# Performance work log

Measured on AMD Instinct MI355X. Metric: run time of the kernel, lower is better.

The kernel has to match this reference:

```python
import math
import jax, jax.numpy as jnp
import numpy as np

NUM_EXPERTS = 8
TOP_K = 2
HIDDEN = 1024
INTERMEDIATE = 4096
CAPACITY_FACTOR = 1.0


def setup_inputs() -> dict:
    key = jax.random.key(0)
    k1, k2, k3, k4, k5, k6 = jax.random.split(key, 6)
    T = 8192
    hidden_states = jax.random.normal(k1, (T, HIDDEN), dtype=jnp.float32)
    # router affinities (already softmax-normalized in the real pipeline; uniform here is fine for correctness)
    expert_affinities = jax.random.uniform(k2, (T, NUM_EXPERTS), dtype=jnp.float32)
    expert_index = jax.random.randint(k3, (T, TOP_K), 0, NUM_EXPERTS, dtype=jnp.int32)
    scale = 0.02
    gate_w = jax.random.normal(k4, (NUM_EXPERTS, HIDDEN, INTERMEDIATE), dtype=jnp.float32) * scale
    up_w = jax.random.normal(k5, (NUM_EXPERTS, HIDDEN, INTERMEDIATE), dtype=jnp.float32) * scale
    down_w = jax.random.normal(k6, (NUM_EXPERTS, INTERMEDIATE, HIDDEN), dtype=jnp.float32) * scale
    return {"hidden_states": hidden_states, "expert_affinities": expert_affinities,
            "gate_w": gate_w, "up_w": up_w, "down_w": down_w, "expert_index": expert_index}


def reference(hidden_states, expert_affinities, gate_w, up_w, down_w, expert_index):
    T, H = hidden_states.shape
    E, K = NUM_EXPERTS, TOP_K
    C = min(math.ceil(T * K * CAPACITY_FACTOR / E), T)  # expert capacity (static)

    # top_k-hot expert mask (T, E)
    expert_mask = jax.nn.one_hot(expert_index, E, dtype=jnp.float32).sum(axis=1)
    # 1-indexed position of each token within each expert's queue
    position_in_expert = jnp.cumsum(expert_mask, axis=0)
    # capacity-based token dropping
    expert_mask = jnp.where(position_in_expert > C, 0.0, expert_mask)

    # masked (and L1-normalized) affinities of chosen experts
    aff_masked = jnp.where(expert_mask == 0, 0.0, expert_affinities)
    denom = jnp.maximum(jnp.sum(jnp.abs(aff_masked), axis=1, keepdims=True), 1e-12)
    aff_masked = aff_masked / denom  # normalize_top_k_affinities=True

    # flattened slot index per (token, expert): expert e occupies slots [e*C, (e+1)*C)
    offsets = jnp.arange(E, dtype=jnp.float32) * C
    pos_off = position_in_expert + offsets[None, :]
    pos_off = jnp.where(expert_mask == 0, 0.0, pos_off)

    # (T, K) slot index (1-based; 0 == dropped)
    perm_idx = jnp.take_along_axis(pos_off, expert_index, axis=1).astype(jnp.int32)

    # invert permutation: slot -> token (1-based; slot 0 collects all dropped tokens, then discarded)
    tok_ids = jnp.broadcast_to((jnp.arange(T, dtype=jnp.int32) + 1)[:, None], (T, K)).reshape(-1)
    assign = jnp.zeros(E * C + 1, dtype=jnp.int32).at[perm_idx.reshape(-1)].set(tok_ids)
    assign = assign[1:].reshape(E, C) - 1
    assign = jnp.maximum(assign, 0)          # empty slots read token 0 (output unused)
    perm_idx = jnp.maximum(perm_idx - 1, 0)  # dropped tokens read slot 0 (affinity == 0)

    # gather tokens into per-expert blocks and run grouped GLU MLP
    x_e = hidden_states[assign]  # (E, C, H)
    gate = jax.nn.silu(jnp.einsum('ech,ehi->eci', x_e, gate_w))
    inter = gate * jnp.einsum('ech,ehi->eci', x_e, up_w)  # (E, C, I)
    out_e = jnp.einsum('eci,eih->ech', inter, down_w)      # (E, C, H)
    permuted_output = out_e.reshape(E * C, H)

    # combine: gather each token's top_k expert outputs weighted by masked affinities
    out_k = permuted_output[perm_idx]                                   # (T, K, H)
    aff_k = jnp.take_along_axis(aff_masked, expert_index, axis=1)       # (T, K)
    return jnp.sum(out_k * aff_k[:, :, None], axis=1)
```

## Files before the change

kernel.cpp:

```cpp
#include <hip/hip_runtime.h>
#include <stdint.h>

#define T_TOK 8192
#define HID   1024
#define INTER 4096
#define NE    8
#define TOPK  2
#define CAP   2048
#define EC    (NE * CAP)


typedef __attribute__((ext_vector_type(8))) short bf16x8;
typedef __attribute__((ext_vector_type(4))) float f32x4;

static __device__ __forceinline__ unsigned short f2bf(float f) {
    union { float f; unsigned u; } a; a.f = f;
    unsigned r = a.u + 0x7FFFu + ((a.u >> 16) & 1u);
    return (unsigned short)(r >> 16);
}
static __device__ __forceinline__ float bf2f(unsigned short b) {
    union { unsigned u; float f; } a; a.u = ((unsigned)b) << 16;
    return a.f;
}

static __device__ __forceinline__ void gload(const unsigned short* g, unsigned short* l) {
    __builtin_amdgcn_global_load_lds((__attribute__((address_space(1))) void*)(uintptr_t)g,
                                     (__attribute__((address_space(3))) void*)l, 16, 0, 0);
}

#define BAR() do { asm volatile("" ::: "memory"); __builtin_amdgcn_s_barrier(); asm volatile("" ::: "memory"); } while (0)
#define WAITVM(N) asm volatile("s_waitcnt vmcnt(" #N ")" ::: "memory")

__global__ __launch_bounds__(512) void route_kernel(const int* __restrict__ eidx,
                                                    int* __restrict__ perm,
                                                    int* __restrict__ assign) {
    int tid = threadIdx.x;
    for (int i = tid; i < EC; i += 512) assign[i] = 0;
    __syncthreads();
    int e = tid >> 6;
    int lane = tid & 63;
    const int TPL = T_TOK / 64;
    int t0 = lane * TPL;
    int cnt = 0;
    for (int t = t0; t < t0 + TPL; ++t) {
        int e0 = eidx[t * 2], e1 = eidx[t * 2 + 1];
        cnt += (e0 == e) + (e1 == e);
    }
    int incl = cnt;
    #pragma unroll
    for (int off = 1; off < 64; off <<= 1) {
        int n = __shfl_up(incl, off, 64);
        if (lane >= off) incl += n;
    }
    int run = incl - cnt;
    for (int t = t0; t < t0 + TPL; ++t) {
        int e0 = eidx[t * 2], e1 = eidx[t * 2 + 1];
        int c = (e0 == e) + (e1 == e);
        if (c) {
            run += c;
            int pos = run;
            bool keep = (pos <= CAP);
            int pi = keep ? (pos + e * CAP) : 0;
            if (e0 == e) perm[t * 2]     = pi;
            if (e1 == e) perm[t * 2 + 1] = pi;
            if (keep) assign[pi - 1] = t;
        }
    }
}

__global__ __launch_bounds__(256) void transpose_cvt2(const float* __restrict__ in0,
                                                      unsigned short* __restrict__ out0,
                                                      const float* __restrict__ in1,
                                                      unsigned short* __restrict__ out1) {
    __shared__ unsigned short tile[64][68];
    int z = blockIdx.z;
    const float* in = (z < 8) ? in0 : in1;
    unsigned short* out = (z < 8) ? out0 : out1;
    int e = z & 7;
    const int R = HID, Cc = INTER;
    const float* inp = in + (size_t)e * R * Cc;
    unsigned short* outp = out + (size_t)e * R * Cc;
    int c0 = blockIdx.x * 64, r0 = blockIdx.y * 64;
    int t = threadIdx.x;
    int x = t & 15;
    int ry = t >> 4;
    #pragma unroll
    for (int j = 0; j < 4; ++j) {
        int row = ry + 16 * j;
        float4 v = *(const float4*)(inp + (size_t)(r0 + row) * Cc + c0 + 4 * x);
        ushort4 o;
        o.x = f2bf(v.x); o.y = f2bf(v.y); o.z = f2bf(v.z); o.w = f2bf(v.w);
        *(ushort4*)&tile[row][4 * x] = o;
    }
    __syncthreads();
    #pragma unroll
    for (int j = 0; j < 4; ++j) {
        int oc = ry + 16 * j;
        ushort4 o;
        o.x = tile[4 * x + 0][oc];
        o.y = tile[4 * x + 1][oc];
        o.z = tile[4 * x + 2][oc];
        o.w = tile[4 * x + 3][oc];
        *(ushort4*)(outp + (size_t)(c0 + oc) * R + r0 + 4 * x) = o;
    }
}

__global__ __launch_bounds__(256) void transpose_cvt(const float* __restrict__ in,
                                                     unsigned short* __restrict__ out,
                                                     int R, int Cc) {
    __shared__ unsigned short tile[64][68];
    int e = blockIdx.z;
    const float* inp = in + (size_t)e * R * Cc;
    unsigned short* outp = out + (size_t)e * R * Cc;
    int c0 = blockIdx.x * 64, r0 = blockIdx.y * 64;
    int t = threadIdx.x;
    int x = t & 15;
    int ry = t >> 4;
    #pragma unroll
    for (int j = 0; j < 4; ++j) {
        int row = ry + 16 * j;
        float4 v = *(const float4*)(inp + (size_t)(r0 + row) * Cc + c0 + 4 * x);
        ushort4 o;
        o.x = f2bf(v.x); o.y = f2bf(v.y); o.z = f2bf(v.z); o.w = f2bf(v.w);
        *(ushort4*)&tile[row][4 * x] = o;
    }
    __syncthreads();
    #pragma unroll
    for (int j = 0; j < 4; ++j) {
        int oc = ry + 16 * j;
        ushort4 o;
        o.x = tile[4 * x + 0][oc];
        o.y = tile[4 * x + 1][oc];
        o.z = tile[4 * x + 2][oc];
        o.w = tile[4 * x + 3][oc];
        *(ushort4*)(outp + (size_t)(c0 + oc) * R + r0 + 4 * x) = o;
    }
}

__global__ __launch_bounds__(256) void gather_cvt(const float* __restrict__ hs,
                                                  const int* __restrict__ assign,
                                                  unsigned short* __restrict__ xe) {
    int s = blockIdx.x;
    int tok = assign[s];
    const float* src = hs + (size_t)tok * HID;
    unsigned short* dst = xe + (size_t)s * HID;
    int h = threadIdx.x * 4;
    float4 v = *(const float4*)(src + h);
    ushort4 o;
    o.x = f2bf(v.x); o.y = f2bf(v.y); o.z = f2bf(v.z); o.w = f2bf(v.w);
    *(ushort4*)(dst + h) = o;
}


#define BUFE 12288

#define MFMA16(ACC, O, B0, B1) \
    _Pragma("unroll") \
    for (int mi = 0; mi < 8; ++mi) { \
        ACC[mi][O]     = __builtin_amdgcn_mfma_f32_16x16x32_bf16(aF[mi], B0, ACC[mi][O], 0, 0, 0); \
        ACC[mi][O + 1] = __builtin_amdgcn_mfma_f32_16x16x32_bf16(aF[mi], B1, ACC[mi][O + 1], 0, 0, 0); \
    }

#define LOAD_AF(rd) \
    _Pragma("unroll") \
    for (int mi = 0; mi < 8; ++mi) aF[mi] = *(const bf16x8*)((rd) + aRd + mi * 512);

__global__ __launch_bounds__(256, 2) void gateup_gemm(const unsigned short* __restrict__ Xe,
                                                      const unsigned short* __restrict__ WgT,
                                                      const unsigned short* __restrict__ WuT,
                                                      unsigned short* __restrict__ interB) {
    extern __shared__ __align__(16) unsigned short smemU[];
    const int K = HID;
    const int NT = K / 32;

    int e  = blockIdx.x;
    int m0 = blockIdx.y * 256;
    int n0 = blockIdx.z * 64;

    int tid = threadIdx.x;
    int lane = tid & 63, w = tid >> 6;
    int lm = lane & 15, hi = lane >> 4;
    int wm = w >> 1, wn = w & 1;

    const int swz  = (hi ^ ((lm >> 1) & 3)) << 3;
    const int aRd  = (wm * 128 + lm) * 32 + swz;
    const int r1Rd = 8192  + (wn * 32 + lm) * 32 + swz;
    const int r2Rd = 10240 + (wn * 32 + lm) * 32 + swz;

    int sr = lane >> 2;
    int sc = ((lane & 3) ^ ((lane >> 3) & 3)) << 3;
    const unsigned short* aS = Xe  + ((size_t)e * CAP   + m0 + w * 64 + sr) * K + sc;
    const unsigned short* gS = WgT + ((size_t)e * INTER + n0 + w * 16 + sr) * K + sc;
    const unsigned short* uS = WuT + ((size_t)e * INTER + n0 + w * 16 + sr) * K + sc;
    const int dA = w * 2048;
    const int dG = 8192  + w * 512;
    const int dU = 10240 + w * 512;

    f32x4 zero = {0.f, 0.f, 0.f, 0.f};
    f32x4 accG[8][2], accU[8][2];
    #pragma unroll
    for (int i = 0; i < 8; ++i) {
        accG[i][0] = zero; accG[i][1] = zero;
        accU[i][0] = zero; accU[i][1] = zero;
    }

    unsigned short* p0 = smemU;
    unsigned short* p1 = smemU + BUFE;
    unsigned short* p2 = smemU + 2 * BUFE;

    {
        #pragma unroll
        for (int j = 0; j < 4; ++j) gload(aS + (size_t)j * 16 * K, p0 + dA + j * 512);
        gload(gS, p0 + dG); gload(uS, p0 + dU);
        #pragma unroll
        for (int j = 0; j < 4; ++j) gload(aS + (size_t)j * 16 * K + 32, p1 + dA + j * 512);
        gload(gS + 32, p1 + dG); gload(uS + 32, p1 + dU);
        WAITVM(6);
        BAR();
    }

    bf16x8 aF[8];
    int gk = 64;
    for (int t = 0; t < NT - 2; ++t) {
        const unsigned short* rd = p0;
        unsigned short* wr = p2;
        LOAD_AF(rd);
        bf16x8 g0 = *(const bf16x8*)(rd + r1Rd);
        bf16x8 g1 = *(const bf16x8*)(rd + r1Rd + 512);
        bf16x8 u0 = *(const bf16x8*)(rd + r2Rd);
        bf16x8 u1 = *(const bf16x8*)(rd + r2Rd + 512);
        #pragma unroll
        for (int j = 0; j < 4; ++j) gload(aS + (size_t)j * 16 * K + gk, wr + dA + j * 512);
        gload(gS + gk, wr + dG);
        gload(uS + gk, wr + dU);
        WAITVM(6);
        BAR();
        __builtin_amdgcn_s_setprio(1);
        MFMA16(accG, 0, g0, g1);
        MFMA16(accU, 0, u0, u1);
        __builtin_amdgcn_s_setprio(0);
        BAR();
        unsigned short* tmp = p0; p0 = p1; p1 = p2; p2 = tmp;
        gk += 32;
    }
    {
        const unsigned short* rd = p0;
        LOAD_AF(rd);
        bf16x8 g0 = *(const bf16x8*)(rd + r1Rd);
        bf16x8 g1 = *(const bf16x8*)(rd + r1Rd + 512);
        bf16x8 u0 = *(const bf16x8*)(rd + r2Rd);
        bf16x8 u1 = *(const bf16x8*)(rd + r2Rd + 512);
        WAITVM(0);
        BAR();
        MFMA16(accG, 0, g0, g1);
        MFMA16(accU, 0, u0, u1);
        BAR();
    }
    {
        const unsigned short* rd = p1;
        LOAD_AF(rd);
        bf16x8 g0 = *(const bf16x8*)(rd + r1Rd);
        bf16x8 g1 = *(const bf16x8*)(rd + r1Rd + 512);
        bf16x8 u0 = *(const bf16x8*)(rd + r2Rd);
        bf16x8 u1 = *(const bf16x8*)(rd + r2Rd + 512);
        MFMA16(accG, 0, g0, g1);
        MFMA16(accU, 0, u0, u1);
    }

    __syncthreads();
    unsigned short* bounce = smemU;
    #pragma unroll
    for (int mi = 0; mi < 8; ++mi)
        #pragma unroll
        for (int nf = 0; nf < 2; ++nf) {
            f32x4 g4 = accG[mi][nf], u4 = accU[mi][nf];
            #pragma unroll
            for (int r = 0; r < 4; ++r) {
                int row = wm * 128 + mi * 16 + (lane >> 4) * 4 + r;
                int col = wn * 32 + nf * 16 + lm;
                float g = g4[r];
                float s = g / (1.f + __expf(-g)) * u4[r];
                bounce[row * 72 + col] = f2bf(s);
            }
        }
    __syncthreads();
    {
        unsigned short* Op = interB + ((size_t)e * CAP + m0) * INTER + n0;
        int rr = tid >> 3, cc = (tid & 7) * 8;
        #pragma unroll
        for (int j = 0; j < 8; ++j) {
            int row = rr + 32 * j;
            bf16x8 v = *(const bf16x8*)&bounce[row * 72 + cc];
            *(bf16x8*)(Op + (size_t)row * INTER + cc) = v;
        }
    }
}

__global__ __launch_bounds__(256, 2) void down_gemm(const unsigned short* __restrict__ interB,
                                                    const unsigned short* __restrict__ WdT,
                                                    unsigned short* __restrict__ pout) {
    extern __shared__ __align__(16) unsigned short smemU[];
    const int K = INTER;
    const int NT = K / 32;

    int e  = blockIdx.x;
    int m0 = blockIdx.y * 256;
    int n0 = blockIdx.z * 128;

    int tid = threadIdx.x;
    int lane = tid & 63, w = tid >> 6;
    int lm = lane & 15, hi = lane >> 4;
    int wm = w >> 1, wn = w & 1;

    const int swz  = (hi ^ ((lm >> 1) & 3)) << 3;
    const int aRd  = (wm * 128 + lm) * 32 + swz;
    const int r1Rd = 8192  + (wn * 32 + lm) * 32 + swz;
    const int r2Rd = 10240 + (wn * 32 + lm) * 32 + swz;

    int sr = lane >> 2;
    int sc = ((lane & 3) ^ ((lane >> 3) & 3)) << 3;
    const unsigned short* aS = interB + ((size_t)e * CAP + m0 + w * 64 + sr) * K + sc;
    int rb1 = (w >> 1) * 64 + (w & 1) * 16;
    const unsigned short* b1S = WdT + ((size_t)e * HID + n0 + rb1 + sr) * K + sc;
    const unsigned short* b2S = WdT + ((size_t)e * HID + n0 + rb1 + 32 + sr) * K + sc;
    const int dA = w * 2048;
    const int d1 = 8192  + w * 512;
    const int d2 = 10240 + w * 512;

    f32x4 zero = {0.f, 0.f, 0.f, 0.f};
    f32x4 acc[8][4];
    #pragma unroll
    for (int i = 0; i < 8; ++i)
        #pragma unroll
        for (int j = 0; j < 4; ++j) acc[i][j] = zero;

    unsigned short* p0 = smemU;
    unsigned short* p1 = smemU + BUFE;
    unsigned short* p2 = smemU + 2 * BUFE;

    {
        #pragma unroll
        for (int j = 0; j < 4; ++j) gload(aS + (size_t)j * 16 * K, p0 + dA + j * 512);
        gload(b1S, p0 + d1); gload(b2S, p0 + d2);
        #pragma unroll
        for (int j = 0; j < 4; ++j) gload(aS + (size_t)j * 16 * K + 32, p1 + dA + j * 512);
        gload(b1S + 32, p1 + d1); gload(b2S + 32, p1 + d2);
        WAITVM(6);
        BAR();
    }

    bf16x8 aF[8];
    int gk = 64;
    for (int t = 0; t < NT - 2; ++t) {
        const unsigned short* rd = p0;
        unsigned short* wr = p2;
        LOAD_AF(rd);
        bf16x8 b0 = *(const bf16x8*)(rd + r1Rd);
        bf16x8 b1 = *(const bf16x8*)(rd + r1Rd + 512);
        bf16x8 b2 = *(const bf16x8*)(rd + r2Rd);
        bf16x8 b3 = *(const bf16x8*)(rd + r2Rd + 512);
        #pragma unroll
        for (int j = 0; j < 4; ++j) gload(aS + (size_t)j * 16 * K + gk, wr + dA + j * 512);
        gload(b1S + gk, wr + d1);
        gload(b2S + gk, wr + d2);
        WAITVM(6);
        BAR();
        __builtin_amdgcn_s_setprio(1);
        MFMA16(acc, 0, b0, b1);
        MFMA16(acc, 2, b2, b3);
        __builtin_amdgcn_s_setprio(0);
        BAR();
        unsigned short* tmp = p0; p0 = p1; p1 = p2; p2 = tmp;
        gk += 32;
    }
    {
        const unsigned short* rd = p0;
        LOAD_AF(rd);
        bf16x8 b0 = *(const bf16x8*)(rd + r1Rd);
        bf16x8 b1 = *(const bf16x8*)(rd + r1Rd + 512);
        bf16x8 b2 = *(const bf16x8*)(rd + r2Rd);
        bf16x8 b3 = *(const bf16x8*)(rd + r2Rd + 512);
        WAITVM(0);
        BAR();
        MFMA16(acc, 0, b0, b1);
        MFMA16(acc, 2, b2, b3);
        BAR();
    }
    {
        const unsigned short* rd = p1;
        LOAD_AF(rd);
        bf16x8 b0 = *(const bf16x8*)(rd + r1Rd);
        bf16x8 b1 = *(const bf16x8*)(rd + r1Rd + 512);
        bf16x8 b2 = *(const bf16x8*)(rd + r2Rd);
        bf16x8 b3 = *(const bf16x8*)(rd + r2Rd + 512);
        MFMA16(acc, 0, b0, b1);
        MFMA16(acc, 2, b2, b3);
    }

    unsigned short* bounce = smemU;
    unsigned short* Op = pout + ((size_t)e * CAP + m0) * HID + n0;
    int rr = tid >> 3, c8 = tid & 7;
    int colp = c8 * 8;
    #pragma unroll
    for (int R = 0; R < 2; ++R) {
        __syncthreads();
        #pragma unroll
        for (int mi = 0; mi < 8; ++mi)
            #pragma unroll
            for (int nf = 0; nf < 2; ++nf) {
                f32x4 a4 = acc[mi][2 * R + nf];
                #pragma unroll
                for (int r = 0; r < 4; ++r) {
                    int row = wm * 128 + mi * 16 + hi * 4 + r;
                    int col = wn * 32 + nf * 16 + lm;
                    bounce[row * 72 + col] = f2bf(a4[r]);
                }
            }
        __syncthreads();
        int gcol = (colp >> 5) * 64 + R * 32 + (colp & 31);
        #pragma unroll
        for (int j = 0; j < 8; ++j) {
            int row = rr + 32 * j;
            bf16x8 v = *(const bf16x8*)&bounce[row * 72 + colp];
            *(bf16x8*)(Op + (size_t)row * HID + gcol) = v;
        }
    }
}

__global__ __launch_bounds__(256) void combine_kernel(const float* __restrict__ aff,
                                                      const int* __restrict__ eidx,
                                                      const int* __restrict__ perm,
                                                      const unsigned short* __restrict__ pout,
                                                      float* __restrict__ out) {
    int t = blockIdx.x;
    int e0 = eidx[t * 2], e1 = eidx[t * 2 + 1];
    int p0 = perm[t * 2], p1 = perm[t * 2 + 1];
    bool k0 = p0 > 0, k1 = p1 > 0;
    float a0 = aff[t * NE + e0], a1 = aff[t * NE + e1];
    float denom = (k0 ? fabsf(a0) : 0.f) + ((e1 != e0 && k1) ? fabsf(a1) : 0.f);
    denom = fmaxf(denom, 1e-12f);
    float w0 = k0 ? a0 / denom : 0.f;
    float w1 = k1 ? a1 / denom : 0.f;
    int s0 = k0 ? p0 - 1 : 0;
    int s1 = k1 ? p1 - 1 : 0;
    int h = threadIdx.x * 4;
    ushort4 v0 = *(const ushort4*)(pout + (size_t)s0 * HID + h);
    ushort4 v1 = *(const ushort4*)(pout + (size_t)s1 * HID + h);
    float4 o;
    o.x = w0 * bf2f(v0.x) + w1 * bf2f(v1.x);
    o.y = w0 * bf2f(v0.y) + w1 * bf2f(v1.y);
    o.z = w0 * bf2f(v0.z) + w1 * bf2f(v1.z);
    o.w = w0 * bf2f(v0.w) + w1 * bf2f(v1.w);
    *(float4*)(out + (size_t)t * HID + h) = o;
}

extern "C" void kernel_launch(void* const* d_in, const int* in_sizes, int n_in,
                              void* d_out, int out_size, void* d_ws, size_t ws_size,
                              hipStream_t stream) {
    (void)in_sizes; (void)n_in; (void)out_size; (void)ws_size;
    const float* hs   = (const float*)d_in[0];
    const float* aff  = (const float*)d_in[1];
    const float* gw   = (const float*)d_in[2];
    const float* uw   = (const float*)d_in[3];
    const float* dw   = (const float*)d_in[4];
    const int*   eidx = (const int*)d_in[5];
    float* out = (float*)d_out;

    char* ws = (char*)d_ws;
    unsigned short* WgT    = (unsigned short*)(ws);
    unsigned short* WuT    = (unsigned short*)(ws + ((size_t)64  << 20));
    unsigned short* WdT    = (unsigned short*)(ws + ((size_t)128 << 20));
    unsigned short* Xe     = (unsigned short*)(ws + ((size_t)192 << 20));
    unsigned short* interB = (unsigned short*)(ws + ((size_t)224 << 20));
    unsigned short* pout   = (unsigned short*)(ws + ((size_t)352 << 20));
    int*            perm   = (int*)           (ws + ((size_t)416 << 20));
    int*            assign = perm + (T_TOK * TOPK);

    static int attr_set = 0;
    if (!attr_set) {
        (void)hipFuncSetAttribute((const void*)gateup_gemm,
                                  hipFuncAttributeMaxDynamicSharedMemorySize, 73728);
        (void)hipFuncSetAttribute((const void*)down_gemm,
                                  hipFuncAttributeMaxDynamicSharedMemorySize, 73728);
        attr_set = 1;
    }

    route_kernel<<<1, 512, 0, stream>>>(eidx, perm, assign);
    transpose_cvt2<<<dim3(INTER / 64, HID / 64, 16), 256, 0, stream>>>(uw, WuT, gw, WgT);
    transpose_cvt<<<dim3(HID / 64, INTER / 64, NE), 256, 0, stream>>>(dw, WdT, INTER, HID);
    gather_cvt<<<EC, 256, 0, stream>>>(hs, assign, Xe);
    gateup_gemm<<<dim3(8, 8, 64), 256, 73728, stream>>>(Xe, WgT, WuT, interB);
    down_gemm<<<dim3(8, 8, 8), 256, 73728, stream>>>(interB, WdT, pout);
    combine_kernel<<<T_TOK, 256, 0, stream>>>(aff, eidx, perm, pout, out);
}
```

Baseline: 911.5 us.

## Load A operand directly to registers, stage only weights through LDS

```diff
diff --git a/kernel.cpp b/kernel.cpp
--- a/kernel.cpp
+++ b/kernel.cpp
@@ -152,19 +152,6 @@
 }
 
 
-#define BUFE 12288
-
-#define MFMA16(ACC, O, B0, B1) \
-    _Pragma("unroll") \
-    for (int mi = 0; mi < 8; ++mi) { \
-        ACC[mi][O]     = __builtin_amdgcn_mfma_f32_16x16x32_bf16(aF[mi], B0, ACC[mi][O], 0, 0, 0); \
-        ACC[mi][O + 1] = __builtin_amdgcn_mfma_f32_16x16x32_bf16(aF[mi], B1, ACC[mi][O + 1], 0, 0, 0); \
-    }
-
-#define LOAD_AF(rd) \
-    _Pragma("unroll") \
-    for (int mi = 0; mi < 8; ++mi) aF[mi] = *(const bf16x8*)((rd) + aRd + mi * 512);
-
 __global__ __launch_bounds__(256, 2) void gateup_gemm(const unsigned short* __restrict__ Xe,
                                                       const unsigned short* __restrict__ WgT,
                                                       const unsigned short* __restrict__ WuT,
@@ -183,18 +170,15 @@
     int wm = w >> 1, wn = w & 1;
 
     const int swz  = (hi ^ ((lm >> 1) & 3)) << 3;
-    const int aRd  = (wm * 128 + lm) * 32 + swz;
-    const int r1Rd = 8192  + (wn * 32 + lm) * 32 + swz;
-    const int r2Rd = 10240 + (wn * 32 + lm) * 32 + swz;
+    const int bOff = (wn * 32 + lm) * 32 + swz;
 
     int sr = lane >> 2;
     int sc = ((lane & 3) ^ ((lane >> 3) & 3)) << 3;
-    const unsigned short* aS = Xe  + ((size_t)e * CAP   + m0 + w * 64 + sr) * K + sc;
     const unsigned short* gS = WgT + ((size_t)e * INTER + n0 + w * 16 + sr) * K + sc;
     const unsigned short* uS = WuT + ((size_t)e * INTER + n0 + w * 16 + sr) * K + sc;
-    const int dA = w * 2048;
-    const int dG = 8192  + w * 512;
-    const int dU = 10240 + w * 512;
+    const int dW = w * 512;
+
+    const unsigned short* aP = Xe + ((size_t)e * CAP + m0 + wm * 128 + lm) * K + hi * 8;
 
     f32x4 zero = {0.f, 0.f, 0.f, 0.f};
     f32x4 accG[8][2], accU[8][2];
@@ -204,68 +188,84 @@
         accU[i][0] = zero; accU[i][1] = zero;
     }
 
-    unsigned short* p0 = smemU;
-    unsigned short* p1 = smemU + BUFE;
-    unsigned short* p2 = smemU + 2 * BUFE;
-
+    int bR = 0, bM = 4096, bS = 8192;
+    bf16x8 aC[8], aN[8];
+
+    gload(gS,      smemU + bR + dW);  gload(uS,      smemU + bR + 2048 + dW);
+    gload(gS + 32, smemU + bM + dW);  gload(uS + 32, smemU + bM + 2048 + dW);
+    #pragma unroll
+    for (int mi = 0; mi < 8; ++mi) aC[mi] = *(const bf16x8*)(aP + mi * 16 * K);
+    WAITVM(10);
+    BAR();
+
+#define GU_TILE(AC, AN, tkc) \
+    { \
+        gload(gS + (tkc) + 64, smemU + bS + dW); \
+        gload(uS + (tkc) + 64, smemU + bS + 2048 + dW); \
+        _Pragma("unroll") \
+        for (int mi = 0; mi < 8; ++mi) \
+            AN[mi] = *(const bf16x8*)(aP + mi * 16 * K + (tkc) + 32); \
+        WAITVM(10); \
+        BAR(); \
+        { \
+            bf16x8 g0 = *(const bf16x8*)(smemU + bR + bOff); \
+            bf16x8 g1 = *(const bf16x8*)(smemU + bR + bOff + 512); \
+            bf16x8 u0 = *(const bf16x8*)(smemU + bR + 2048 + bOff); \
+            bf16x8 u1 = *(const bf16x8*)(smemU + bR + 2048 + bOff + 512); \
+            __builtin_amdgcn_s_setprio(1); \
+            _Pragma("unroll") \
+            for (int mi = 0; mi < 8; ++mi) { \
+                accG[mi][0] = __builtin_amdgcn_mfma_f32_16x16x32_bf16(AC[mi], g0, accG[mi][0], 0, 0, 0); \
+                accG[mi][1] = __builtin_amdgcn_mfma_f32_16x16x32_bf16(AC[mi], g1, accG[mi][1], 0, 0, 0); \
+                accU[mi][0] = __builtin_amdgcn_mfma_f32_16x16x32_bf16(AC[mi], u0, accU[mi][0], 0, 0, 0); \
+                accU[mi][1] = __builtin_amdgcn_mfma_f32_16x16x32_bf16(AC[mi], u1, accU[mi][1], 0, 0, 0); \
+            } \
+            __builtin_amdgcn_s_setprio(0); \
+        } \
+        BAR(); \
+        int _bt = bR; bR = bM; bM = bS; bS = _bt; \
+    }
+
+    int tk = 0;
+    for (int t = 0; t < NT - 2; t += 2) {
+        GU_TILE(aC, aN, tk);
+        GU_TILE(aN, aC, tk + 32);
+        tk += 64;
+    }
     {
         #pragma unroll
-        for (int j = 0; j < 4; ++j) gload(aS + (size_t)j * 16 * K, p0 + dA + j * 512);
-        gload(gS, p0 + dG); gload(uS, p0 + dU);
-        #pragma unroll
-        for (int j = 0; j < 4; ++j) gload(aS + (size_t)j * 16 * K + 32, p1 + dA + j * 512);
-        gload(gS + 32, p1 + dG); gload(uS + 32, p1 + dU);
-        WAITVM(6);
+        for (int mi = 0; mi < 8; ++mi) aN[mi] = *(const bf16x8*)(aP + mi * 16 * K + tk + 32);
+        WAITVM(8);
         BAR();
-    }
-
-    bf16x8 aF[8];
-    int gk = 64;
-    for (int t = 0; t < NT - 2; ++t) {
-        const unsigned short* rd = p0;
-        unsigned short* wr = p2;
-        LOAD_AF(rd);
-        bf16x8 g0 = *(const bf16x8*)(rd + r1Rd);
-        bf16x8 g1 = *(const bf16x8*)(rd + r1Rd + 512);
-        bf16x8 u0 = *(const bf16x8*)(rd + r2Rd);
-        bf16x8 u1 = *(const bf16x8*)(rd + r2Rd + 512);
-        #pragma unroll
-        for (int j = 0; j < 4; ++j) gload(aS + (size_t)j * 16 * K + gk, wr + dA + j * 512);
-        gload(gS + gk, wr + dG);
-        gload(uS + gk, wr + dU);
-        WAITVM(6);
+        bf16x8 g0 = *(const bf16x8*)(smemU + bR + bOff);
+        bf16x8 g1 = *(const bf16x8*)(smemU + bR + bOff + 512);
+        bf16x8 u0 = *(const bf16x8*)(smemU + bR + 2048 + bOff);
+        bf16x8 u1 = *(const bf16x8*)(smemU + bR + 2048 + bOff + 512);
+        #pragma unroll
+        for (int mi = 0; mi < 8; ++mi) {
+            accG[mi][0] = __builtin_amdgcn_mfma_f32_16x16x32_bf16(aC[mi], g0, accG[mi][0], 0, 0, 0);
+            accG[mi][1] = __builtin_amdgcn_mfma_f32_16x16x32_bf16(aC[mi], g1, accG[mi][1], 0, 0, 0);
+            accU[mi][0] = __builtin_amdgcn_mfma_f32_16x16x32_bf16(aC[mi], u0, accU[mi][0], 0, 0, 0);
+            accU[mi][1] = __builtin_amdgcn_mfma_f32_16x16x32_bf16(aC[mi], u1, accU[mi][1], 0, 0, 0);
+        }
         BAR();
-        __builtin_amdgcn_s_setprio(1);
-        MFMA16(accG, 0, g0, g1);
-        MFMA16(accU, 0, u0, u1);
-        __builtin_amdgcn_s_setprio(0);
-        BAR();
-        unsigned short* tmp = p0; p0 = p1; p1 = p2; p2 = tmp;
-        gk += 32;
+        int _bt = bR; bR = bM; bM = bS; bS = _bt;
     }
     {
-        const unsigned short* rd = p0;
-        LOAD_AF(rd);
-        bf16x8 g0 = *(const bf16x8*)(rd + r1Rd);
-        bf16x8 g1 = *(const bf16x8*)(rd + r1Rd + 512);
-        bf16x8 u0 = *(const bf16x8*)(rd + r2Rd);
-        bf16x8 u1 = *(const bf16x8*)(rd + r2Rd + 512);
         WAITVM(0);
-        BAR();
-        MFMA16(accG, 0, g0, g1);
-        MFMA16(accU, 0, u0, u1);
-        BAR();
-    }
-    {
-        const unsigned short* rd = p1;
-        LOAD_AF(rd);
-        bf16x8 g0 = *(const bf16x8*)(rd + r1Rd);
-        bf16x8 g1 = *(const bf16x8*)(rd + r1Rd + 512);
-        bf16x8 u0 = *(const bf16x8*)(rd + r2Rd);
-        bf16x8 u1 = *(const bf16x8*)(rd + r2Rd + 512);
-        MFMA16(accG, 0, g0, g1);
-        MFMA16(accU, 0, u0, u1);
-    }
+        bf16x8 g0 = *(const bf16x8*)(smemU + bR + bOff);
+        bf16x8 g1 = *(const bf16x8*)(smemU + bR + bOff + 512);
+        bf16x8 u0 = *(const bf16x8*)(smemU + bR + 2048 + bOff);
+        bf16x8 u1 = *(const bf16x8*)(smemU + bR + 2048 + bOff + 512);
+        #pragma unroll
+        for (int mi = 0; mi < 8; ++mi) {
+            accG[mi][0] = __builtin_amdgcn_mfma_f32_16x16x32_bf16(aN[mi], g0, accG[mi][0], 0, 0, 0);
+            accG[mi][1] = __builtin_amdgcn_mfma_f32_16x16x32_bf16(aN[mi], g1, accG[mi][1], 0, 0, 0);
+            accU[mi][0] = __builtin_amdgcn_mfma_f32_16x16x32_bf16(aN[mi], u0, accU[mi][0], 0, 0, 0);
+            accU[mi][1] = __builtin_amdgcn_mfma_f32_16x16x32_bf16(aN[mi], u1, accU[mi][1], 0, 0, 0);
+        }
+    }
+#undef GU_TILE
 
     __syncthreads();
     unsigned short* bounce = smemU;
@@ -276,7 +276,7 @@
             f32x4 g4 = accG[mi][nf], u4 = accU[mi][nf];
             #pragma unroll
             for (int r = 0; r < 4; ++r) {
-                int row = wm * 128 + mi * 16 + (lane >> 4) * 4 + r;
+                int row = wm * 128 + mi * 16 + hi * 4 + r;
                 int col = wn * 32 + nf * 16 + lm;
                 float g = g4[r];
                 float s = g / (1.f + __expf(-g)) * u4[r];
@@ -304,8 +304,8 @@
     const int NT = K / 32;
 
     int e  = blockIdx.x;
-    int m0 = blockIdx.y * 256;
-    int n0 = blockIdx.z * 128;
+    int n0 = blockIdx.y * 128;
+    int m0 = blockIdx.z * 256;
 
     int tid = threadIdx.x;
     int lane = tid & 63, w = tid >> 6;
@@ -313,19 +313,16 @@
     int wm = w >> 1, wn = w & 1;
 
     const int swz  = (hi ^ ((lm >> 1) & 3)) << 3;
-    const int aRd  = (wm * 128 + lm) * 32 + swz;
-    const int r1Rd = 8192  + (wn * 32 + lm) * 32 + swz;
-    const int r2Rd = 10240 + (wn * 32 + lm) * 32 + swz;
+    const int bOff = (wn * 32 + lm) * 32 + swz;
 
     int sr = lane >> 2;
     int sc = ((lane & 3) ^ ((lane >> 3) & 3)) << 3;
-    const unsigned short* aS = interB + ((size_t)e * CAP + m0 + w * 64 + sr) * K + sc;
     int rb1 = (w >> 1) * 64 + (w & 1) * 16;
     const unsigned short* b1S = WdT + ((size_t)e * HID + n0 + rb1 + sr) * K + sc;
     const unsigned short* b2S = WdT + ((size_t)e * HID + n0 + rb1 + 32 + sr) * K + sc;
-    const int dA = w * 2048;
-    const int d1 = 8192  + w * 512;
-    const int d2 = 10240 + w * 512;
+    const int dW = w * 512;
+
+    const unsigned short* aP = interB + ((size_t)e * CAP + m0 + wm * 128 + lm) * K + hi * 8;
 
     f32x4 zero = {0.f, 0.f, 0.f, 0.f};
     f32x4 acc[8][4];
@@ -334,68 +331,84 @@
         #pragma unroll
         for (int j = 0; j < 4; ++j) acc[i][j] = zero;
 
-    unsigned short* p0 = smemU;
-    unsigned short* p1 = smemU + BUFE;
-    unsigned short* p2 = smemU + 2 * BUFE;
-
+    int bR = 0, bM = 4096, bS = 8192;
+    bf16x8 aC[8], aN[8];
+
+    gload(b1S,      smemU + bR + dW);  gload(b2S,      smemU + bR + 2048 + dW);
+    gload(b1S + 32, smemU + bM + dW);  gload(b2S + 32, smemU + bM + 2048 + dW);
+    #pragma unroll
+    for (int mi = 0; mi < 8; ++mi) aC[mi] = *(const bf16x8*)(aP + mi * 16 * K);
+    WAITVM(10);
+    BAR();
+
+#define DN_TILE(AC, AN, tkc) \
+    { \
+        gload(b1S + (tkc) + 64, smemU + bS + dW); \
+        gload(b2S + (tkc) + 64, smemU + bS + 2048 + dW); \
+        _Pragma("unroll") \
+        for (int mi = 0; mi < 8; ++mi) \
+            AN[mi] = *(const bf16x8*)(aP + mi * 16 * K + (tkc) + 32); \
+        WAITVM(10); \
+        BAR(); \
+        { \
+            bf16x8 b0 = *(const bf16x8*)(smemU + bR + bOff); \
+            bf16x8 b1 = *(const bf16x8*)(smemU + bR + bOff + 512); \
+            bf16x8 b2 = *(const bf16x8*)(smemU + bR + 2048 + bOff); \
+            bf16x8 b3 = *(const bf16x8*)(smemU + bR + 2048 + bOff + 512); \
+            __builtin_amdgcn_s_setprio(1); \
+            _Pragma("unroll") \
+            for (int mi = 0; mi < 8; ++mi) { \
+                acc[mi][0] = __builtin_amdgcn_mfma_f32_16x16x32_bf16(AC[mi], b0, acc[mi][0], 0, 0, 0); \
+                acc[mi][1] = __builtin_amdgcn_mfma_f32_16x16x32_bf16(AC[mi], b1, acc[mi][1], 0, 0, 0); \
+                acc[mi][2] = __builtin_amdgcn_mfma_f32_16x16x32_bf16(AC[mi], b2, acc[mi][2], 0, 0, 0); \
+                acc[mi][3] = __builtin_amdgcn_mfma_f32_16x16x32_bf16(AC[mi], b3, acc[mi][3], 0, 0, 0); \
+            } \
+            __builtin_amdgcn_s_setprio(0); \
+        } \
+        BAR(); \
+        int _bt = bR; bR = bM; bM = bS; bS = _bt; \
+    }
+
+    int tk = 0;
+    for (int t = 0; t < NT - 2; t += 2) {
+        DN_TILE(aC, aN, tk);
+        DN_TILE(aN, aC, tk + 32);
+        tk += 64;
+    }
     {
         #pragma unroll
-        for (int j = 0; j < 4; ++j) gload(aS + (size_t)j * 16 * K, p0 + dA + j * 512);
-        gload(b1S, p0 + d1); gload(b2S, p0 + d2);
-        #pragma unroll
-        for (int j = 0; j < 4; ++j) gload(aS + (size_t)j * 16 * K + 32, p1 + dA + j * 512);
-        gload(b1S + 32, p1 + d1); gload(b2S + 32, p1 + d2);
-        WAITVM(6);
+        for (int mi = 0; mi < 8; ++mi) aN[mi] = *(const bf16x8*)(aP + mi * 16 * K + tk + 32);
+        WAITVM(8);
         BAR();
-    }
-
-    bf16x8 aF[8];
-    int gk = 64;
-    for (int t = 0; t < NT - 2; ++t) {
-        const unsigned short* rd = p0;
-        unsigned short* wr = p2;
-        LOAD_AF(rd);
-        bf16x8 b0 = *(const bf16x8*)(rd + r1Rd);
-        bf16x8 b1 = *(const bf16x8*)(rd + r1Rd + 512);
-        bf16x8 b2 = *(const bf16x8*)(rd + r2Rd);
-        bf16x8 b3 = *(const bf16x8*)(rd + r2Rd + 512);
-        #pragma unroll
-        for (int j = 0; j < 4; ++j) gload(aS + (size_t)j * 16 * K + gk, wr + dA + j * 512);
-        gload(b1S + gk, wr + d1);
-        gload(b2S + gk, wr + d2);
-        WAITVM(6);
+        bf16x8 b0 = *(const bf16x8*)(smemU + bR + bOff);
+        bf16x8 b1 = *(const bf16x8*)(smemU + bR + bOff + 512);
+        bf16x8 b2 = *(const bf16x8*)(smemU + bR + 2048 + bOff);
+        bf16x8 b3 = *(const bf16x8*)(smemU + bR + 2048 + bOff + 512);
+        #pragma unroll
+        for (int mi = 0; mi < 8; ++mi) {
+            acc[mi][0] = __builtin_amdgcn_mfma_f32_16x16x32_bf16(aC[mi], b0, acc[mi][0], 0, 0, 0);
+            acc[mi][1] = __builtin_amdgcn_mfma_f32_16x16x32_bf16(aC[mi], b1, acc[mi][1], 0, 0, 0);
+            acc[mi][2] = __builtin_amdgcn_mfma_f32_16x16x32_bf16(aC[mi], b2, acc[mi][2], 0, 0, 0);
+            acc[mi][3] = __builtin_amdgcn_mfma_f32_16x16x32_bf16(aC[mi], b3, acc[mi][3], 0, 0, 0);
+        }
         BAR();
-        __builtin_amdgcn_s_setprio(1);
-        MFMA16(acc, 0, b0, b1);
-        MFMA16(acc, 2, b2, b3);
-        __builtin_amdgcn_s_setprio(0);
-        BAR();
-        unsigned short* tmp = p0; p0 = p1; p1 = p2; p2 = tmp;
-        gk += 32;
+        int _bt = bR; bR = bM; bM = bS; bS = _bt;
     }
     {
-        const unsigned short* rd = p0;
-        LOAD_AF(rd);
-        bf16x8 b0 = *(const bf16x8*)(rd + r1Rd);
-        bf16x8 b1 = *(const bf16x8*)(rd + r1Rd + 512);
-        bf16x8 b2 = *(const bf16x8*)(rd + r2Rd);
-        bf16x8 b3 = *(const bf16x8*)(rd + r2Rd + 512);
         WAITVM(0);
-        BAR();
-        MFMA16(acc, 0, b0, b1);
-        MFMA16(acc, 2, b2, b3);
-        BAR();
-    }
-    {
-        const unsigned short* rd = p1;
-        LOAD_AF(rd);
-        bf16x8 b0 = *(const bf16x8*)(rd + r1Rd);
-        bf16x8 b1 = *(const bf16x8*)(rd + r1Rd + 512);
-        bf16x8 b2 = *(const bf16x8*)(rd + r2Rd);
-        bf16x8 b3 = *(const bf16x8*)(rd + r2Rd + 512);
-        MFMA16(acc, 0, b0, b1);
-        MFMA16(acc, 2, b2, b3);
-    }
+        bf16x8 b0 = *(const bf16x8*)(smemU + bR + bOff);
+        bf16x8 b1 = *(const bf16x8*)(smemU + bR + bOff + 512);
+        bf16x8 b2 = *(const bf16x8*)(smemU + bR + 2048 + bOff);
+        bf16x8 b3 = *(const bf16x8*)(smemU + bR + 2048 + bOff + 512);
+        #pragma unroll
+        for (int mi = 0; mi < 8; ++mi) {
+            acc[mi][0] = __builtin_amdgcn_mfma_f32_16x16x32_bf16(aN[mi], b0, acc[mi][0], 0, 0, 0);
+            acc[mi][1] = __builtin_amdgcn_mfma_f32_16x16x32_bf16(aN[mi], b1, acc[mi][1], 0, 0, 0);
+            acc[mi][2] = __builtin_amdgcn_mfma_f32_16x16x32_bf16(aN[mi], b2, acc[mi][2], 0, 0, 0);
+            acc[mi][3] = __builtin_amdgcn_mfma_f32_16x16x32_bf16(aN[mi], b3, acc[mi][3], 0, 0, 0);
+        }
+    }
+#undef DN_TILE
 
     unsigned short* bounce = smemU;
     unsigned short* Op = pout + ((size_t)e * CAP + m0) * HID + n0;
@@ -479,9 +492,9 @@
     static int attr_set = 0;
     if (!attr_set) {
         (void)hipFuncSetAttribute((const void*)gateup_gemm,
-                                  hipFuncAttributeMaxDynamicSharedMemorySize, 73728);
+                                  hipFuncAttributeMaxDynamicSharedMemorySize, 36864);
         (void)hipFuncSetAttribute((const void*)down_gemm,
-                                  hipFuncAttributeMaxDynamicSharedMemorySize, 73728);
+                                  hipFuncAttributeMaxDynamicSharedMemorySize, 36864);
         attr_set = 1;
     }
 
@@ -489,7 +502,7 @@
     transpose_cvt2<<<dim3(INTER / 64, HID / 64, 16), 256, 0, stream>>>(uw, WuT, gw, WgT);
     transpose_cvt<<<dim3(HID / 64, INTER / 64, NE), 256, 0, stream>>>(dw, WdT, INTER, HID);
     gather_cvt<<<EC, 256, 0, stream>>>(hs, assign, Xe);
-    gateup_gemm<<<dim3(8, 8, 64), 256, 73728, stream>>>(Xe, WgT, WuT, interB);
-    down_gemm<<<dim3(8, 8, 8), 256, 73728, stream>>>(interB, WdT, pout);
+    gateup_gemm<<<dim3(8, 8, 64), 256, 36864, stream>>>(Xe, WgT, WuT, interB);
+    down_gemm<<<dim3(8, 8, 8), 256, 36864, stream>>>(interB, WdT, pout);
     combine_kernel<<<T_TOK, 256, 0, stream>>>(aff, eidx, perm, pout, out);
 }
```

After: 1.325 ms. 45.3% more time.
